# Kernel tuning notes

Measured on AMD Instinct MI355X. Metric: run time of the kernel, lower is better.

Reference implementation:

```python
import jax, jax.numpy as jnp
import numpy as np

B, N, C_IN, HID, K, DEG = 8192, 64, 128, 128, 5, 8


def setup_inputs() -> dict:
    key = jax.random.key(0)
    ks = jax.random.split(key, 8)
    total = B * N
    E = B * N * DEG
    x = jax.random.normal(ks[0], (total, C_IN), dtype=jnp.float32)
    batch = jnp.repeat(jnp.arange(B, dtype=jnp.int64), N)
    g = jnp.repeat(jnp.arange(B, dtype=jnp.int64), N * DEG)
    src = g * N + jax.random.randint(ks[1], (E,), 0, N).astype(jnp.int64)
    dst = g * N + jax.random.randint(ks[2], (E,), 0, N).astype(jnp.int64)
    edge_index = jnp.stack([src, dst])  # [2, E]
    s = 0.05
    return {
        "x": x,
        "edge_index": edge_index,
        "batch": batch,
        "W_pool": jax.random.normal(ks[3], (C_IN, K), dtype=jnp.float32) * s,
        "b_pool": jnp.zeros((K,), jnp.float32),
        "W1": jax.random.normal(ks[4], (C_IN, HID), dtype=jnp.float32) * s,
        "b1": jnp.zeros((HID,), jnp.float32),
        "W2": jax.random.normal(ks[5], (HID, HID), dtype=jnp.float32) * s,
        "b2": jnp.zeros((HID,), jnp.float32),
        "W_lin": jax.random.normal(ks[6], (HID, 1), dtype=jnp.float32) * s,
        "b_lin": jnp.zeros((1,), jnp.float32),
        "num_graphs": B,
        "max_nodes": N,
    }


def dense_gcn(x, adj, W, b, mask=None):
    # PyG DenseGCNConv with add_loop=True: diagonal set to 1 on a copy
    n = adj.shape[1]
    idx = jnp.arange(n)
    adj_l = adj.at[:, idx, idx].set(1.0)
    out = x @ W  # [B, n, out]
    d = jnp.clip(adj_l.sum(-1), 1.0) ** -0.5  # [B, n]
    adj_n = d[:, :, None] * adj_l * d[:, None, :]
    out = jnp.einsum('bnm,bmc->bnc', adj_n, out) + b
    if mask is not None:
        out = out * mask[..., None]
    return out


def reference(x, edge_index, batch, W_pool, b_pool, W1, b1, W2, b2, W_lin, b_lin,
              num_graphs, max_nodes):
    total = x.shape[0]
    # to_dense_batch: position of each node within its graph (batch is sorted)
    first_idx = jax.ops.segment_min(jnp.arange(total), batch, num_segments=num_graphs)
    pos = jnp.arange(total) - first_idx[batch]
    x_dense = jnp.zeros((num_graphs, max_nodes, x.shape[1]), x.dtype).at[batch, pos].set(x)
    mask = jnp.zeros((num_graphs, max_nodes), x.dtype).at[batch, pos].set(1.0)
    # to_dense_adj
    src, dst = edge_index[0], edge_index[1]
    adj = jnp.zeros((num_graphs, max_nodes, max_nodes), x.dtype)
    adj = adj.at[batch[src], pos[src], pos[dst]].add(1.0)

    s = dense_gcn(x_dense, adj, W_pool, b_pool, mask)       # [B, N, K]
    x_l1 = dense_gcn(x_dense, adj, W1, b1, mask)            # [B, N, H]

    # dense_diff_pool (losses are discarded by the original forward)
    s = jax.nn.softmax(s, axis=-1) * mask[..., None]
    xm = x_l1 * mask[..., None]
    x_p1 = jnp.einsum('bnk,bnc->bkc', s, xm)                # [B, K, H]
    adj_p1 = jnp.einsum('bnk,bnm,bml->bkl', s, adj, s)      # [B, K, K]

    x_l2 = dense_gcn(x_p1, adj_p1, W2, b2)                  # [B, K, H]
    pooled = x_l2.sum(axis=1)                               # global_add_pool -> [B, H]
    return pooled @ W_lin + b_lin                           # [B, 1]
```

## Files before the change

kernel.cpp:

```cpp
#include <hip/hip_runtime.h>
#include <hip/hip_bf16.h>

#define NN 64
#define CI 128
#define HD 128
#define KC 5
#define AJW 17

#define WS_WC  0
#define WS_B1Z 768
#define WS_B2W 769

extern "C" __global__ void zprep(const float* __restrict__ W1,
                                 const float* __restrict__ Wp,
                                 const float* __restrict__ W2,
                                 const float* __restrict__ Wl,
                                 const float* __restrict__ b1,
                                 const float* __restrict__ b2,
                                 float* __restrict__ ws)
{
    const int t = threadIdx.x;
    __shared__ float sz_[HD];
    float a0 = 0.f, a1 = 0.f;
    for (int c = 0; c < HD; ++c) {
        const float wl = Wl[c];
        a0 += W2[t * HD + c] * wl;
        a1 += W2[(t + 64) * HD + c] * wl;
    }
    sz_[t] = a0; sz_[t + 64] = a1;
    float p1 = b1[t] * a0 + b1[t + 64] * a1;
    float p2 = b2[t] * Wl[t] + b2[t + 64] * Wl[t + 64];
    #pragma unroll
    for (int off = 32; off; off >>= 1) {
        p1 += __shfl_down(p1, off, 64);
        p2 += __shfl_down(p2, off, 64);
    }
    if (t == 0) { ws[WS_B1Z] = p1; ws[WS_B2W] = p2; }
    __syncthreads();
    #pragma unroll
    for (int rr = 0; rr < 2; ++rr) {
        const int r = t + rr * 64;
        float acc = 0.f;
        for (int h2 = 0; h2 < HD; ++h2) acc += W1[r * HD + h2] * sz_[h2];
        #pragma unroll
        for (int k = 0; k < KC; ++k) ws[WS_WC + r * 6 + k] = Wp[r * KC + k];
        ws[WS_WC + r * 6 + 5] = acc;
    }
}

extern "C" __global__ __launch_bounds__(256, 6)
void diffpool_main(const float* __restrict__ x,
                   const int* __restrict__ ei,
                   const float* __restrict__ bp,
                   const float* __restrict__ bl,
                   const float* __restrict__ ws,
                   float* __restrict__ out,
                   int E, int epg)
{
    __shared__ unsigned int sadjb[NN][AJW];
    __shared__ float sA [4][NN * KC];
    __shared__ float sBu[4][NN * KC];
    __shared__ float sc [4][NN];
    __shared__ float spp[4][25];
    __shared__ float sSm[NN][6];
    __shared__ float sq[NN];
    __shared__ float sd[NN];
    __shared__ unsigned int srdeg[NN];
    __shared__ float sadjp[25];
    __shared__ float sd2[KC];
    __shared__ float scoef[KC];

    const int t = threadIdx.x;
    const int g = blockIdx.x;
    const int lane = t & 63;
    const int wv = t >> 6;
    const int ch = t & 15;
    const int n = lane;
    const int h = wv;

    const float bp0 = bp[0], bp1 = bp[1], bp2 = bp[2], bp3 = bp[3], bp4 = bp[4];
    const float c_b1z = ws[WS_B1Z], c_b2w = ws[WS_B2W], c_bl = bl[0];

    int e0s = -1, e0d = 0, e1s = -1, e1d = 0;
    const int base = g * epg;
    if (t < epg)       { e0s = ei[base + t] & 63;        e0d = ei[E + base + t] & 63; }
    if (t + 256 < epg) { e1s = ei[base + t + 256] & 63;  e1d = ei[E + base + t + 256] & 63; }

    {
        unsigned int* ap = &sadjb[0][0];
        for (int i = t; i < NN * AJW; i += 256) ap[i] = 0u;
        if (t < NN) srdeg[t] = 0u;
    }
    __syncthreads();

    {
        if (e0s >= 0) {
            atomicAdd(&sadjb[e0s][e0d >> 2], 1u << ((e0d & 3) * 8));
            atomicAdd(&srdeg[e0s], 1u);
        }
        if (e1s >= 0) {
            atomicAdd(&sadjb[e1s][e1d >> 2], 1u << ((e1d & 3) * 8));
            atomicAdd(&srdeg[e1s], 1u);
        }
        for (int j = t + 512; j < epg; j += 256) {
            const int sn = ei[base + j] & 63;
            const int dn = ei[E + base + j] & 63;
            atomicAdd(&sadjb[sn][dn >> 2], 1u << ((dn & 3) * 8));
            atomicAdd(&srdeg[sn], 1u);
        }
        float wc[48];
        {
            const float4* wc4 = reinterpret_cast<const float4*>(ws + WS_WC + ch * 48);
            #pragma unroll
            for (int i4 = 0; i4 < 12; ++i4)
                *reinterpret_cast<float4*>(&wc[i4 * 4]) = wc4[i4];
        }
        const float* xg = x + (size_t)g * (NN * CI);
        #pragma unroll
        for (int i = 0; i < 4; ++i) {
            const int row = (t >> 4) + 16 * i;
            const float* xr = xg + row * CI + ch * 8;
            const float4 v0 = *reinterpret_cast<const float4*>(xr);
            const float4 v1 = *reinterpret_cast<const float4*>(xr + 4);
            float acc[6];
            #pragma unroll
            for (int k = 0; k < 6; ++k) acc[k] = 0.f;
            #pragma unroll
            for (int k = 0; k < 6; ++k) {
                acc[k] += v0.x * wc[0 * 6 + k] + v0.y * wc[1 * 6 + k]
                        + v0.z * wc[2 * 6 + k] + v0.w * wc[3 * 6 + k]
                        + v1.x * wc[4 * 6 + k] + v1.y * wc[5 * 6 + k]
                        + v1.z * wc[6 * 6 + k] + v1.w * wc[7 * 6 + k];
            }
            #pragma unroll
            for (int k = 0; k < 6; ++k) {
                float r = acc[k];
                r += __shfl_xor(r, 1, 16);
                r += __shfl_xor(r, 2, 16);
                r += __shfl_xor(r, 4, 16);
                r += __shfl_xor(r, 8, 16);
                acc[k] = r;
            }
            float val = acc[0];
            #pragma unroll
            for (int k = 1; k < 6; ++k) val = (ch == k) ? acc[k] : val;
            if (ch < KC)       sSm[row][ch] = val;
            else if (ch == 5)  sq[row] = val;
        }
    }
    __syncthreads();

    unsigned aw0, aw1, aw2, aw3;
    float dlane;
    {
        const unsigned selfb = (sadjb[lane][lane >> 2] >> ((lane & 3) * 8)) & 255u;
        dlane = rsqrtf((float)(srdeg[lane] + 1u - selfb));
        sd[lane] = dlane;
        aw0 = sadjb[n][h * 4 + 0];
        aw1 = sadjb[n][h * 4 + 1];
        aw2 = sadjb[n][h * 4 + 2];
        aw3 = sadjb[n][h * 4 + 3];
        float a0 = 0.f, a1 = 0.f, a2 = 0.f, a3 = 0.f, a4 = 0.f, cp = 0.f;
        #pragma unroll
        for (int i = 0; i < 4; ++i) {
            const unsigned w = (i == 0) ? aw0 : (i == 1) ? aw1 : (i == 2) ? aw2 : aw3;
            #pragma unroll
            for (int bb = 0; bb < 4; ++bb) {
                const int m = h * 16 + i * 4 + bb;
                const float al = (m == n) ? 1.f : (float)((w >> (bb * 8)) & 255u);
                const float f = al * sd[m];
                a0 += f * sSm[m][0]; a1 += f * sSm[m][1]; a2 += f * sSm[m][2];
                a3 += f * sSm[m][3]; a4 += f * sSm[m][4];
                cp += f * sq[m];
            }
        }
        float* pp = &sA[h][n * KC];
        pp[0] = a0; pp[1] = a1; pp[2] = a2; pp[3] = a3; pp[4] = a4;
        sc[h][n] = cp;
    }
    __syncthreads();

    float s0v, s1v, s2v, s3v, s4v;
    {
        float a0 = sA[0][n*KC+0] + sA[1][n*KC+0] + sA[2][n*KC+0] + sA[3][n*KC+0];
        float a1 = sA[0][n*KC+1] + sA[1][n*KC+1] + sA[2][n*KC+1] + sA[3][n*KC+1];
        float a2 = sA[0][n*KC+2] + sA[1][n*KC+2] + sA[2][n*KC+2] + sA[3][n*KC+2];
        float a3 = sA[0][n*KC+3] + sA[1][n*KC+3] + sA[2][n*KC+3] + sA[3][n*KC+3];
        float a4 = sA[0][n*KC+4] + sA[1][n*KC+4] + sA[2][n*KC+4] + sA[3][n*KC+4];
        a0 = a0 * dlane + bp0; a1 = a1 * dlane + bp1; a2 = a2 * dlane + bp2;
        a3 = a3 * dlane + bp3; a4 = a4 * dlane + bp4;
        const float mx = fmaxf(fmaxf(fmaxf(a0, a1), fmaxf(a2, a3)), a4);
        a0 = expf(a0 - mx); a1 = expf(a1 - mx); a2 = expf(a2 - mx);
        a3 = expf(a3 - mx); a4 = expf(a4 - mx);
        const float inv = 1.f / (a0 + a1 + a2 + a3 + a4);
        s0v = a0 * inv; s1v = a1 * inv; s2v = a2 * inv; s3v = a3 * inv; s4v = a4 * inv;
        sSm[n][0] = s0v; sSm[n][1] = s1v; sSm[n][2] = s2v;
        sSm[n][3] = s3v; sSm[n][4] = s4v;
        float u0 = 0.f, u1 = 0.f, u2 = 0.f, u3 = 0.f, u4 = 0.f;
        #pragma unroll
        for (int i = 0; i < 4; ++i) {
            const unsigned w = (i == 0) ? aw0 : (i == 1) ? aw1 : (i == 2) ? aw2 : aw3;
            #pragma unroll
            for (int bb = 0; bb < 4; ++bb) {
                const int m = h * 16 + i * 4 + bb;
                const float c = (float)((w >> (bb * 8)) & 255u);
                u0 += c * sSm[m][0]; u1 += c * sSm[m][1]; u2 += c * sSm[m][2];
                u3 += c * sSm[m][3]; u4 += c * sSm[m][4];
            }
        }
        float* pp = &sBu[h][n * KC];
        pp[0] = u0; pp[1] = u1; pp[2] = u2; pp[3] = u3; pp[4] = u4;
    }
    __syncthreads();

    if (lane < 25) {
        const int k = lane / 5, l = lane - k * 5;
        float a = 0.f;
        #pragma unroll
        for (int i = 0; i < 16; ++i) {
            const int m = h * 16 + i;
            const float uu = sBu[0][m*KC+l] + sBu[1][m*KC+l]
                           + sBu[2][m*KC+l] + sBu[3][m*KC+l];
            a += sSm[m][k] * uu;
        }
        spp[h][lane] = a;
    }
    __syncthreads();

    {
        if (lane < 25)
            sadjp[lane] = spp[0][lane] + spp[1][lane] + spp[2][lane] + spp[3][lane];
        if (lane < KC) {
            float s_ = 0.f;
            #pragma unroll
            for (int l = 0; l < KC; ++l) s_ += sadjp[lane * KC + l];
            s_ += 1.f - sadjp[lane * 6];
            sd2[lane] = rsqrtf(fmaxf(s_, 1.f));
        }
        if (lane < KC) {
            float a = 0.f;
            #pragma unroll
            for (int k = 0; k < KC; ++k) a += sd2[k] * sadjp[k * KC + lane];
            a += sd2[lane] * (1.f - sadjp[lane * 6]);
            scoef[lane] = sd2[lane] * a;
        }
        const float t5 = scoef[0] * s0v + scoef[1] * s1v + scoef[2] * s2v +
                         scoef[3] * s3v + scoef[4] * s4v;
        const float wn = dlane * t5;
        const float cfull = sc[0][n] + sc[1][n] + sc[2][n] + sc[3][n];
        float cb = t5;
        float v = wn * cfull;
        #pragma unroll
        for (int off = 32; off; off >>= 1) {
            cb += __shfl_down(cb, off, 64);
            v  += __shfl_down(v,  off, 64);
        }
        if (wv == 0 && lane == 0)
            out[g] = v + cb * c_b1z + 5.f * c_b2w + c_bl;
    }
}

extern "C" void kernel_launch(void* const* d_in, const int* in_sizes, int n_in,
                              void* d_out, int out_size, void* d_ws, size_t ws_size,
                              hipStream_t stream) {
    const float* x  = (const float*)d_in[0];
    const int*   ei = (const int*)d_in[1];
    const float* Wp = (const float*)d_in[3];
    const float* bp = (const float*)d_in[4];
    const float* W1 = (const float*)d_in[5];
    const float* b1 = (const float*)d_in[6];
    const float* W2 = (const float*)d_in[7];
    const float* b2 = (const float*)d_in[8];
    const float* Wl = (const float*)d_in[9];
    const float* bl = (const float*)d_in[10];
    float* out = (float*)d_out;
    float* ws  = (float*)d_ws;

    const int B = out_size;
    const int E = in_sizes[1] / 2;
    const int epg = E / B;

    zprep<<<1, 64, 0, stream>>>(W1, Wp, W2, Wl, b1, b2, ws);
    diffpool_main<<<B, 256, 0, stream>>>(x, ei, bp, bl, ws, out, E, epg);
}
```

Measured before the change: 425.6 us.

## Process one graph per wavefront instead of one per block, dropping block barriers

Each 256-thread block now handles four graphs, one per 64-lane wavefront, with per-wave shared adjacency and score buffers, so all __syncthreads and cross-wave partial-sum arrays are removed. The pooled 5x5 adjacency is reduced with wave shuffles, the row degree is computed from packed byte counts instead of a separate atomic degree counter, and edges are loaded as int4 vectors when each graph has 512 edges. The aim is to cut barrier and LDS traffic. In exchange each lane does four times more serial work per graph, and the absence of barriers relies on wavefront-synchronous LDS visibility.

```diff
diff --git a/kernel.cpp b/kernel.cpp
--- a/kernel.cpp
+++ b/kernel.cpp
@@ -1,5 +1,4 @@
 #include <hip/hip_runtime.h>
-#include <hip/hip_bf16.h>
 
 #define NN 64
 #define CI 128
@@ -48,6 +47,9 @@
     }
 }
 
+#define EDGE(sv_, dv_) { const int s_ = (sv_) & 63, d_ = (dv_) & 63; \
+    atomicAdd(&adj[s_][d_ >> 2], 1u << ((d_ & 3) * 8)); }
+
 extern "C" __global__ __launch_bounds__(256, 6)
 void diffpool_main(const float* __restrict__ x,
                    const int* __restrict__ ei,
@@ -55,83 +57,69 @@
                    const float* __restrict__ bl,
                    const float* __restrict__ ws,
                    float* __restrict__ out,
-                   int E, int epg)
+                   int E, int epg, int B)
 {
-    __shared__ unsigned int sadjb[NN][AJW];
-    __shared__ float sA [4][NN * KC];
-    __shared__ float sBu[4][NN * KC];
-    __shared__ float sc [4][NN];
-    __shared__ float spp[4][25];
-    __shared__ float sSm[NN][6];
-    __shared__ float sq[NN];
-    __shared__ float sd[NN];
-    __shared__ unsigned int srdeg[NN];
-    __shared__ float sadjp[25];
-    __shared__ float sd2[KC];
-    __shared__ float scoef[KC];
+    __shared__ __attribute__((aligned(16))) unsigned int sadjb[4][NN][AJW];
+    __shared__ __attribute__((aligned(16))) float sSm[4][NN][8];
 
     const int t = threadIdx.x;
-    const int g = blockIdx.x;
     const int lane = t & 63;
     const int wv = t >> 6;
-    const int ch = t & 15;
+    const int g = blockIdx.x * 4 + wv;
+    if (g >= B) return;
+
+    unsigned int (*adj)[AJW] = sadjb[wv];
+    float (*sm)[8] = sSm[wv];
+
     const int n = lane;
-    const int h = wv;
+    const int ch = lane & 15;
+    const int rg = lane >> 4;
 
     const float bp0 = bp[0], bp1 = bp[1], bp2 = bp[2], bp3 = bp[3], bp4 = bp[4];
     const float c_b1z = ws[WS_B1Z], c_b2w = ws[WS_B2W], c_bl = bl[0];
 
-    int e0s = -1, e0d = 0, e1s = -1, e1d = 0;
     const int base = g * epg;
-    if (t < epg)       { e0s = ei[base + t] & 63;        e0d = ei[E + base + t] & 63; }
-    if (t + 256 < epg) { e1s = ei[base + t + 256] & 63;  e1d = ei[E + base + t + 256] & 63; }
-
-    {
-        unsigned int* ap = &sadjb[0][0];
-        for (int i = t; i < NN * AJW; i += 256) ap[i] = 0u;
-        if (t < NN) srdeg[t] = 0u;
-    }
-    __syncthreads();
-
-    {
-        if (e0s >= 0) {
-            atomicAdd(&sadjb[e0s][e0d >> 2], 1u << ((e0d & 3) * 8));
-            atomicAdd(&srdeg[e0s], 1u);
-        }
-        if (e1s >= 0) {
-            atomicAdd(&sadjb[e1s][e1d >> 2], 1u << ((e1d & 3) * 8));
-            atomicAdd(&srdeg[e1s], 1u);
-        }
-        for (int j = t + 512; j < epg; j += 256) {
+    int4 es0, es1, ed0, ed1;
+    const bool fast = (epg == 512);
+    if (fast) {
+        es0 = *reinterpret_cast<const int4*>(ei + base + lane * 8);
+        es1 = *reinterpret_cast<const int4*>(ei + base + lane * 8 + 4);
+        ed0 = *reinterpret_cast<const int4*>(ei + E + base + lane * 8);
+        ed1 = *reinterpret_cast<const int4*>(ei + E + base + lane * 8 + 4);
+    }
+
+    #pragma unroll
+    for (int i = 0; i < AJW; ++i) adj[lane][i] = 0u;
+
+    if (fast) {
+        EDGE(es0.x, ed0.x); EDGE(es0.y, ed0.y); EDGE(es0.z, ed0.z); EDGE(es0.w, ed0.w);
+        EDGE(es1.x, ed1.x); EDGE(es1.y, ed1.y); EDGE(es1.z, ed1.z); EDGE(es1.w, ed1.w);
+    } else {
+        for (int j = lane; j < epg; j += 64) {
             const int sn = ei[base + j] & 63;
             const int dn = ei[E + base + j] & 63;
-            atomicAdd(&sadjb[sn][dn >> 2], 1u << ((dn & 3) * 8));
-            atomicAdd(&srdeg[sn], 1u);
-        }
+            atomicAdd(&adj[sn][dn >> 2], 1u << ((dn & 3) * 8));
+        }
+    }
+
+    {
         float wc[48];
-        {
-            const float4* wc4 = reinterpret_cast<const float4*>(ws + WS_WC + ch * 48);
-            #pragma unroll
-            for (int i4 = 0; i4 < 12; ++i4)
-                *reinterpret_cast<float4*>(&wc[i4 * 4]) = wc4[i4];
-        }
+        const float4* wc4 = reinterpret_cast<const float4*>(ws + WS_WC + ch * 48);
+        #pragma unroll
+        for (int i4 = 0; i4 < 12; ++i4)
+            *reinterpret_cast<float4*>(&wc[i4 * 4]) = wc4[i4];
         const float* xg = x + (size_t)g * (NN * CI);
-        #pragma unroll
-        for (int i = 0; i < 4; ++i) {
-            const int row = (t >> 4) + 16 * i;
+        #pragma unroll 4
+        for (int i = 0; i < 16; ++i) {
+            const int row = rg + 4 * i;
             const float* xr = xg + row * CI + ch * 8;
             const float4 v0 = *reinterpret_cast<const float4*>(xr);
             const float4 v1 = *reinterpret_cast<const float4*>(xr + 4);
             float acc[6];
             #pragma unroll
-            for (int k = 0; k < 6; ++k) acc[k] = 0.f;
-            #pragma unroll
-            for (int k = 0; k < 6; ++k) {
-                acc[k] += v0.x * wc[0 * 6 + k] + v0.y * wc[1 * 6 + k]
-                        + v0.z * wc[2 * 6 + k] + v0.w * wc[3 * 6 + k]
-                        + v1.x * wc[4 * 6 + k] + v1.y * wc[5 * 6 + k]
-                        + v1.z * wc[6 * 6 + k] + v1.w * wc[7 * 6 + k];
-            }
+            for (int k = 0; k < 6; ++k)
+                acc[k] = v0.x * wc[0*6+k] + v0.y * wc[1*6+k] + v0.z * wc[2*6+k] + v0.w * wc[3*6+k]
+                       + v1.x * wc[4*6+k] + v1.y * wc[5*6+k] + v1.z * wc[6*6+k] + v1.w * wc[7*6+k];
             #pragma unroll
             for (int k = 0; k < 6; ++k) {
                 float r = acc[k];
@@ -144,120 +132,113 @@
             float val = acc[0];
             #pragma unroll
             for (int k = 1; k < 6; ++k) val = (ch == k) ? acc[k] : val;
-            if (ch < KC)       sSm[row][ch] = val;
-            else if (ch == 5)  sq[row] = val;
-        }
-    }
-    __syncthreads();
-
-    unsigned aw0, aw1, aw2, aw3;
-    float dlane;
+            if (ch < 6)      sm[row][ch] = val;
+            else if (ch < 8) sm[row][ch] = 0.f;
+        }
+    }
+
+    unsigned w[16];
+    #pragma unroll
+    for (int i = 0; i < 16; ++i) w[i] = adj[n][i];
+    unsigned acc1 = 0u, acc2 = 0u;
+    #pragma unroll
+    for (int i = 0; i < 16; ++i) {
+        acc1 += w[i] & 0x00FF00FFu;
+        acc2 += (w[i] >> 8) & 0x00FF00FFu;
+    }
+    const unsigned rowsum = (acc1 & 0xFFFFu) + (acc1 >> 16) + (acc2 & 0xFFFFu) + (acc2 >> 16);
+    const unsigned selfb = (adj[n][n >> 2] >> ((n & 3) * 8)) & 255u;
+    const float dlane = rsqrtf((float)(rowsum + 1u - selfb));
+    sm[n][6] = dlane;
+
+    float a0 = 0.f, a1 = 0.f, a2 = 0.f, a3 = 0.f, a4 = 0.f, cp = 0.f;
+    #pragma unroll
+    for (int i = 0; i < 16; ++i) {
+        #pragma unroll
+        for (int b = 0; b < 4; ++b) {
+            const int m = i * 4 + b;
+            float al = (float)((w[i] >> (b * 8)) & 255u);
+            al = (m == n) ? 1.f : al;
+            const float4 s01 = *reinterpret_cast<const float4*>(&sm[m][0]);
+            const float4 s23 = *reinterpret_cast<const float4*>(&sm[m][4]);
+            const float f = al * s23.z;
+            a0 += f * s01.x; a1 += f * s01.y; a2 += f * s01.z; a3 += f * s01.w;
+            a4 += f * s23.x;
+            cp += f * s23.y;
+        }
+    }
+
+    a0 = a0 * dlane + bp0; a1 = a1 * dlane + bp1; a2 = a2 * dlane + bp2;
+    a3 = a3 * dlane + bp3; a4 = a4 * dlane + bp4;
+    const float mx = fmaxf(fmaxf(fmaxf(a0, a1), fmaxf(a2, a3)), a4);
+    a0 = expf(a0 - mx); a1 = expf(a1 - mx); a2 = expf(a2 - mx);
+    a3 = expf(a3 - mx); a4 = expf(a4 - mx);
+    const float inv = 1.f / (a0 + a1 + a2 + a3 + a4);
+    float sv[5];
+    sv[0] = a0 * inv; sv[1] = a1 * inv; sv[2] = a2 * inv; sv[3] = a3 * inv; sv[4] = a4 * inv;
     {
-        const unsigned selfb = (sadjb[lane][lane >> 2] >> ((lane & 3) * 8)) & 255u;
-        dlane = rsqrtf((float)(srdeg[lane] + 1u - selfb));
-        sd[lane] = dlane;
-        aw0 = sadjb[n][h * 4 + 0];
-        aw1 = sadjb[n][h * 4 + 1];
-        aw2 = sadjb[n][h * 4 + 2];
-        aw3 = sadjb[n][h * 4 + 3];
-        float a0 = 0.f, a1 = 0.f, a2 = 0.f, a3 = 0.f, a4 = 0.f, cp = 0.f;
-        #pragma unroll
-        for (int i = 0; i < 4; ++i) {
-            const unsigned w = (i == 0) ? aw0 : (i == 1) ? aw1 : (i == 2) ? aw2 : aw3;
-            #pragma unroll
-            for (int bb = 0; bb < 4; ++bb) {
-                const int m = h * 16 + i * 4 + bb;
-                const float al = (m == n) ? 1.f : (float)((w >> (bb * 8)) & 255u);
-                const float f = al * sd[m];
-                a0 += f * sSm[m][0]; a1 += f * sSm[m][1]; a2 += f * sSm[m][2];
-                a3 += f * sSm[m][3]; a4 += f * sSm[m][4];
-                cp += f * sq[m];
-            }
-        }
-        float* pp = &sA[h][n * KC];
-        pp[0] = a0; pp[1] = a1; pp[2] = a2; pp[3] = a3; pp[4] = a4;
-        sc[h][n] = cp;
-    }
-    __syncthreads();
-
-    float s0v, s1v, s2v, s3v, s4v;
-    {
-        float a0 = sA[0][n*KC+0] + sA[1][n*KC+0] + sA[2][n*KC+0] + sA[3][n*KC+0];
-        float a1 = sA[0][n*KC+1] + sA[1][n*KC+1] + sA[2][n*KC+1] + sA[3][n*KC+1];
-        float a2 = sA[0][n*KC+2] + sA[1][n*KC+2] + sA[2][n*KC+2] + sA[3][n*KC+2];
-        float a3 = sA[0][n*KC+3] + sA[1][n*KC+3] + sA[2][n*KC+3] + sA[3][n*KC+3];
-        float a4 = sA[0][n*KC+4] + sA[1][n*KC+4] + sA[2][n*KC+4] + sA[3][n*KC+4];
-        a0 = a0 * dlane + bp0; a1 = a1 * dlane + bp1; a2 = a2 * dlane + bp2;
-        a3 = a3 * dlane + bp3; a4 = a4 * dlane + bp4;
-        const float mx = fmaxf(fmaxf(fmaxf(a0, a1), fmaxf(a2, a3)), a4);
-        a0 = expf(a0 - mx); a1 = expf(a1 - mx); a2 = expf(a2 - mx);
-        a3 = expf(a3 - mx); a4 = expf(a4 - mx);
-        const float inv = 1.f / (a0 + a1 + a2 + a3 + a4);
-        s0v = a0 * inv; s1v = a1 * inv; s2v = a2 * inv; s3v = a3 * inv; s4v = a4 * inv;
-        sSm[n][0] = s0v; sSm[n][1] = s1v; sSm[n][2] = s2v;
-        sSm[n][3] = s3v; sSm[n][4] = s4v;
-        float u0 = 0.f, u1 = 0.f, u2 = 0.f, u3 = 0.f, u4 = 0.f;
-        #pragma unroll
-        for (int i = 0; i < 4; ++i) {
-            const unsigned w = (i == 0) ? aw0 : (i == 1) ? aw1 : (i == 2) ? aw2 : aw3;
-            #pragma unroll
-            for (int bb = 0; bb < 4; ++bb) {
-                const int m = h * 16 + i * 4 + bb;
-                const float c = (float)((w >> (bb * 8)) & 255u);
-                u0 += c * sSm[m][0]; u1 += c * sSm[m][1]; u2 += c * sSm[m][2];
-                u3 += c * sSm[m][3]; u4 += c * sSm[m][4];
-            }
-        }
-        float* pp = &sBu[h][n * KC];
-        pp[0] = u0; pp[1] = u1; pp[2] = u2; pp[3] = u3; pp[4] = u4;
-    }
-    __syncthreads();
-
-    if (lane < 25) {
-        const int k = lane / 5, l = lane - k * 5;
+        float4 s01; s01.x = sv[0]; s01.y = sv[1]; s01.z = sv[2]; s01.w = sv[3];
+        *reinterpret_cast<float4*>(&sm[n][0]) = s01;
+        sm[n][4] = sv[4];
+    }
+
+    float uv[5] = {0.f, 0.f, 0.f, 0.f, 0.f};
+    #pragma unroll
+    for (int i = 0; i < 16; ++i) {
+        #pragma unroll
+        for (int b = 0; b < 4; ++b) {
+            const int m = i * 4 + b;
+            const float c = (float)((w[i] >> (b * 8)) & 255u);
+            const float4 s03 = *reinterpret_cast<const float4*>(&sm[m][0]);
+            const float s4r = sm[m][4];
+            uv[0] += c * s03.x; uv[1] += c * s03.y; uv[2] += c * s03.z;
+            uv[3] += c * s03.w; uv[4] += c * s4r;
+        }
+    }
+
+    float pr[25];
+    #pragma unroll
+    for (int k = 0; k < 5; ++k)
+        #pragma unroll
+        for (int l = 0; l < 5; ++l)
+            pr[k * 5 + l] = sv[k] * uv[l];
+    #pragma unroll
+    for (int p = 0; p < 25; ++p) {
+        float r = pr[p];
+        r += __shfl_xor(r, 1, 64);
+        r += __shfl_xor(r, 2, 64);
+        r += __shfl_xor(r, 4, 64);
+        r += __shfl_xor(r, 8, 64);
+        r += __shfl_xor(r, 16, 64);
+        r += __shfl_xor(r, 32, 64);
+        pr[p] = r;
+    }
+
+    float d2[5], cf[5];
+    #pragma unroll
+    for (int k = 0; k < 5; ++k) {
+        float s_ = pr[k*5+0] + pr[k*5+1] + pr[k*5+2] + pr[k*5+3] + pr[k*5+4];
+        s_ += 1.f - pr[k * 6];
+        d2[k] = rsqrtf(fmaxf(s_, 1.f));
+    }
+    #pragma unroll
+    for (int l = 0; l < 5; ++l) {
         float a = 0.f;
         #pragma unroll
-        for (int i = 0; i < 16; ++i) {
-            const int m = h * 16 + i;
-            const float uu = sBu[0][m*KC+l] + sBu[1][m*KC+l]
-                           + sBu[2][m*KC+l] + sBu[3][m*KC+l];
-            a += sSm[m][k] * uu;
-        }
-        spp[h][lane] = a;
-    }
-    __syncthreads();
-
-    {
-        if (lane < 25)
-            sadjp[lane] = spp[0][lane] + spp[1][lane] + spp[2][lane] + spp[3][lane];
-        if (lane < KC) {
-            float s_ = 0.f;
-            #pragma unroll
-            for (int l = 0; l < KC; ++l) s_ += sadjp[lane * KC + l];
-            s_ += 1.f - sadjp[lane * 6];
-            sd2[lane] = rsqrtf(fmaxf(s_, 1.f));
-        }
-        if (lane < KC) {
-            float a = 0.f;
-            #pragma unroll
-            for (int k = 0; k < KC; ++k) a += sd2[k] * sadjp[k * KC + lane];
-            a += sd2[lane] * (1.f - sadjp[lane * 6]);
-            scoef[lane] = sd2[lane] * a;
-        }
-        const float t5 = scoef[0] * s0v + scoef[1] * s1v + scoef[2] * s2v +
-                         scoef[3] * s3v + scoef[4] * s4v;
-        const float wn = dlane * t5;
-        const float cfull = sc[0][n] + sc[1][n] + sc[2][n] + sc[3][n];
-        float cb = t5;
-        float v = wn * cfull;
-        #pragma unroll
-        for (int off = 32; off; off >>= 1) {
-            cb += __shfl_down(cb, off, 64);
-            v  += __shfl_down(v,  off, 64);
-        }
-        if (wv == 0 && lane == 0)
-            out[g] = v + cb * c_b1z + 5.f * c_b2w + c_bl;
-    }
+        for (int k = 0; k < 5; ++k) a += d2[k] * pr[k * 5 + l];
+        a += d2[l] * (1.f - pr[l * 6]);
+        cf[l] = d2[l] * a;
+    }
+    const float t5 = cf[0]*sv[0] + cf[1]*sv[1] + cf[2]*sv[2] + cf[3]*sv[3] + cf[4]*sv[4];
+    float v  = (dlane * t5) * cp;
+    float cb = t5;
+    #pragma unroll
+    for (int off = 32; off; off >>= 1) {
+        v  += __shfl_down(v,  off, 64);
+        cb += __shfl_down(cb, off, 64);
+    }
+    if (lane == 0)
+        out[g] = v + cb * c_b1z + 5.f * c_b2w + c_bl;
 }
 
 extern "C" void kernel_launch(void* const* d_in, const int* in_sizes, int n_in,
@@ -281,5 +262,6 @@
     const int epg = E / B;
 
     zprep<<<1, 64, 0, stream>>>(W1, Wp, W2, Wl, b1, b2, ws);
-    diffpool_main<<<B, 256, 0, stream>>>(x, ei, bp, bl, ws, out, E, epg);
+    const int nb = (B + 3) / 4;
+    diffpool_main<<<nb, 256, 0, stream>>>(x, ei, bp, bl, ws, out, E, epg, B);
 }
```

Result: slower. 456.1 us (+7.2%).
